# Kernel tuning notes

Measured on AMD Instinct MI355X. Metric: run time of the kernel, lower is better.

The kernel has to match this reference:

```python
import jax, jax.numpy as jnp
from jax import lax
import numpy as np

# ----- static optical constants (from config) -----
N = 500            # phase mask grid
PX = 1e-6          # pixel pitch [m]
WL = 532e-9        # wavelength [m]
FL = 0.1           # focal length [m]
RI = 1.0           # refractive index
FWHC = 150e-6      # laser beam FWHC
K = 2.0 * np.pi * RI / WL
QE, DARK_MEAN, READ_STD, GAIN, MAX_ADU = 0.9, 0.005, 1.6, 2.0, 65535.0
MAX_VAL = 4.0e9    # Normalize01 max
PHOTONS = 1.0e6    # photons per emitter (max_intensity-style scaling)
R = 15             # psf_keep_radius -> 31x31 crops

_x = np.arange(-N // 2, N // 2) * PX
_X, _Y = np.meshgrid(_x, _x)
INCIDENT = np.exp(-(_X**2 + _Y**2) / (2.0 * FWHC**2)).astype(np.float32)
_C1 = (np.pi / (WL * FL) * (_X**2 + _Y**2)) % (2.0 * np.pi)
B1 = np.exp(-1j * _C1).astype(np.complex64)
# angular-spectrum gamma, directly in unshifted fft order
_F = np.fft.fftfreq(N, d=PX)
_A, _B = np.meshgrid(RI * WL * _F, RI * WL * _F)
GAMMA = np.sqrt(np.maximum(1.0 - _A**2 - _B**2, 0.0)).astype(np.float32)

def _gauss7():
    m = (7 - 1) / 2.0
    y, x = np.ogrid[-m:m + 1, -m:m + 1]
    h = np.exp(-(x * x + y * y) / 2.0)
    h[h < np.finfo(h.dtype).eps * h.max()] = 0
    return h.astype(np.float32)
GAUSS7 = _gauss7()


def setup_inputs() -> dict:
    key = jax.random.key(0)
    k1, k2, k3, k4, k5, k6, k7 = jax.random.split(key, 7)
    B, Ne = 8, 64
    phase_mask = jax.random.uniform(k1, (N, N), jnp.float32, 0.0, 2.0 * np.pi)
    zs = jax.random.uniform(k2, (Ne,), jnp.float32, 0.0, 1e-4)  # defocus depths [m]
    xyz = jax.random.randint(k3, (B, Ne, 2), 0, 170, jnp.int32) + 15  # in [15,184]
    std_u = jax.random.uniform(k4, (1,), jnp.float32)
    eps_dark = jax.random.normal(k5, (B, 1, 198, 198), jnp.float32)
    eps_photon = jax.random.normal(k6, (B, 1, 198, 198), jnp.float32)
    eps_read = jax.random.normal(k7, (B, 1, 198, 198), jnp.float32)
    return {"phase_mask": phase_mask, "zs": zs, "xyz": xyz, "std_u": std_u,
            "eps_dark": eps_dark, "eps_photon": eps_photon, "eps_read": eps_read}


def _forward(phase_mask, zs, xyz, std_u, eps_dark, eps_photon, eps_read):
    Bn, Ne = xyz.shape[0], xyz.shape[1]
    # --- FFT-based PSF generation (angular spectrum propagation) ---
    field = (INCIDENT * jnp.exp(1j * phase_mask) * B1).astype(jnp.complex64)  # [N,N]
    Ef = jnp.fft.fft2(field)                                                  # [N,N]
    H = jnp.exp(1j * ((K * GAMMA)[None] * zs[:, None, None]))                 # [Ne,N,N]
    Eprop = jnp.fft.ifft2(Ef[None] * H)                                       # [Ne,N,N]
    inten = jnp.abs(Eprop) ** 2
    c = N // 2
    psf = inten[:, c - R:c + R + 1, c - R:c + R + 1]                          # [Ne,31,31]
    psf = psf / (jnp.sum(psf, (-2, -1), keepdims=True) + 1e-12) * PHOTONS
    images4D = jnp.broadcast_to(psf[None], (Bn, Ne, 2 * R + 1, 2 * R + 1))
    # --- imgs4dto3d: scatter-add 31x31 patches into 200x200 canvas ---
    offs = jnp.arange(2 * R + 1) - R
    rows = xyz[..., 0][..., None, None] + offs[None, None, :, None]           # [B,Ne,31,1]
    cols = xyz[..., 1][..., None, None] + offs[None, None, None, :]           # [B,Ne,1,31]
    bidx = jnp.arange(Bn)[:, None, None, None]
    canvas = jnp.zeros((Bn, 200, 200), psf.dtype).at[bidx, rows, cols].add(images4D)
    img = canvas[:, None]                                                     # [B,1,200,200]
    # --- BlurLayer: per-draw std gaussian, conv pad=2 -> 198x198 ---
    std = 0.8 + 0.4 * std_u[0]
    s2 = std * std
    kern = (1.0 / (2.0 * jnp.pi * s2)) * GAUSS7 ** (1.0 / s2)
    blurred = lax.conv_general_dilated(img, kern[None, None], (1, 1),
                                       [(2, 2), (2, 2)],
                                       dimension_numbers=("NCHW", "OIHW", "NCHW"))
    # --- NoiseLayer (reparameterized gaussian approximations) ---
    sig = blurred * QE
    dark = DARK_MEAN + eps_dark * jnp.sqrt(jnp.float32(DARK_MEAN))
    total = jnp.maximum(sig + dark, 0.0)
    noisy = total + eps_photon * jnp.sqrt(jnp.maximum(total, 1e-12))
    elec = noisy + eps_read * READ_STD
    adu = jnp.clip(elec * GAIN, 0.0, MAX_ADU)
    # --- Normalize01 ---
    out = jnp.where(adu <= 10.0, 1.0, jnp.minimum(adu, MAX_VAL)) / MAX_VAL
    return out.astype(jnp.float32)


def reference(phase_mask, zs, xyz, std_u, eps_dark, eps_photon, eps_read):
    return _forward(phase_mask, zs, xyz, std_u, eps_dark, eps_photon, eps_read)
```

## Files before the change

kernel.cpp:

```cpp
#include <hip/hip_runtime.h>
#include <math.h>

#define NN 500
#define NE 64
#define BATCH 8
#define RR 15
#define PW 31
#define CAN 200
#define OHW 198
#define TWO_PI_F 6.28318530717958647692f
#define SETUP_N (BATCH * CAN * CAN + NE + 49)

#define BG2_F16 (64 * 2 * 2 * 64 * 8)
#define ASCALE (1.0f / 64.0f)

using f16x8 = __attribute__((ext_vector_type(8))) _Float16;
using f32x16 = __attribute__((ext_vector_type(16))) float;

__device__ __forceinline__ void fast_sincos_red(float theta, float* s, float* c) {
    const float INV2PI = 0.15915494309189535f;
    const float PI2_HI = 6.28318548202514648f;
    const float PI2_LO = -1.7484556e-7f;
    float n = rintf(theta * INV2PI);
    float r = fmaf(n, -PI2_HI, theta);
    r = fmaf(n, -PI2_LO, r);
    *s = __sinf(r);
    *c = __cosf(r);
}

__global__ void k_setup(const float* __restrict__ std_u,
                        float* __restrict__ kgamma,
                        float2* __restrict__ tw,
                        float* __restrict__ kern,
                        float* __restrict__ canvas,
                        float* __restrict__ psf_sums,
                        _Float16* __restrict__ Bg2) {
    int idx = blockIdx.x * blockDim.x + threadIdx.x;
    if (idx < NN) {
        double th = 2.0 * M_PI * (double)idx / (double)NN;
        tw[idx] = make_float2((float)cos(th), (float)sin(th));
    }
    if (idx < BG2_F16) {
        int e = idx & 7;
        int lane = (idx >> 3) & 63;
        int nt = (idx >> 9) & 1;
        int plane = (idx >> 10) & 1;
        int gs = idx >> 11;
        int kap = gs * 16 + (lane >> 5) * 8 + e;
        int nu = nt * 32 + (lane & 31);
        float outv = 0.f;
        if (kap < 2 * NN) {
            int u = kap >> 1, p = kap & 1;
            int ri = nu >> 1, q = nu & 1;
            int r = 235 + ri;
            int m = (u * r) % NN;
            double th = 2.0 * M_PI * (double)m / (double)NN;
            double wre = cos(th), wim = sin(th);
            double val = (q == 0) ? ((p == 0) ? wre : -wim)
                                  : ((p == 0) ? wim : wre);
            float x = (float)val;
            _Float16 h = (_Float16)x;
            outv = (plane == 0) ? (float)h : (x - (float)h);
        }
        Bg2[idx] = (_Float16)outv;
    }
    if (idx < BATCH * CAN * CAN) canvas[idx] = 0.f;
    if (idx >= BATCH * CAN * CAN && idx < BATCH * CAN * CAN + NE)
        psf_sums[idx - BATCH * CAN * CAN] = 0.f;
    if (idx >= BATCH * CAN * CAN + NE && idx < SETUP_N) {
        int t = idx - (BATCH * CAN * CAN + NE);
        float stdv = 0.8f + 0.4f * std_u[0];
        float s2 = stdv * stdv;
        int a = t / 7 - 3, b = t % 7 - 3;
        float g = (float)exp(-0.5 * (double)(a * a + b * b));
        kern[t] = (1.0f / (2.0f * (float)M_PI * s2)) * powf(g, 1.0f / s2);
    }
    if (idx >= NN * NN) return;
    int i = idx / NN, j = idx % NN;
    double fy = (double)((i < 250) ? i : i - 500) * 2000.0;
    double fx = (double)((j < 250) ? j : j - 500) * 2000.0;
    double a = 5.32e-7 * fx;
    double b = 5.32e-7 * fy;
    double g = 1.0 - a * a - b * b;
    g = (g > 0.0) ? sqrt(g) : 0.0;
    float Kf = (float)(2.0 * M_PI * 1.0 / 5.32e-7);
    kgamma[idx] = Kf * (float)g;
}

__device__ __forceinline__ void ct_dft_stages(const float2* xs, const float2* tts,
                                              float2* S, int t,
                                              float2* out1, float2* out2, int* kout) {
    if (t < 250) {
        int d = t / 25;
        int b = t % 25;
        float2 st = tts[(25 * d) % NN];
        float wr = 1.f, wi = 0.f;
        float Er = 0.f, Ei = 0.f, Or_ = 0.f, Oi = 0.f;
#pragma unroll
        for (int a = 0; a < 20; a += 2) {
            float2 x0 = xs[25 * a + b];
            Er += x0.x * wr - x0.y * wi;
            Ei += x0.x * wi + x0.y * wr;
            float nr = wr * st.x - wi * st.y;
            float ni = wr * st.y + wi * st.x;
            float2 x1 = xs[25 * (a + 1) + b];
            Or_ += x1.x * nr - x1.y * ni;
            Oi  += x1.x * ni + x1.y * nr;
            wr = nr * st.x - ni * st.y;
            wi = nr * st.y + ni * st.x;
        }
        S[b * 21 + d]      = make_float2(Er + Or_, Ei + Oi);
        S[b * 21 + d + 10] = make_float2(Er - Or_, Ei - Oi);
    }
    __syncthreads();
    if (t < 250) {
        int k = t;
        int d1 = k % 20;
        int d2 = (d1 + 10) % 20;
        float2 s1 = tts[k];
        float wr = 1.f, wi = 0.f;
        float a1r = 0.f, a1i = 0.f, a2r = 0.f, a2i = 0.f;
#pragma unroll
        for (int b = 0; b < 25; ++b) {
            float2 u1 = S[b * 21 + d1];
            float2 u2 = S[b * 21 + d2];
            a1r += u1.x * wr - u1.y * wi;
            a1i += u1.x * wi + u1.y * wr;
            float sgnb = (b & 1) ? -1.f : 1.f;
            float w2r = sgnb * wr, w2i = sgnb * wi;
            a2r += u2.x * w2r - u2.y * w2i;
            a2i += u2.x * w2i + u2.y * w2r;
            float nr = wr * s1.x - wi * s1.y;
            wi = wr * s1.y + wi * s1.x;
            wr = nr;
        }
        *out1 = make_float2(a1r, a1i);
        *out2 = make_float2(a2r, a2i);
        *kout = k;
    }
}

__global__ void k_dft_rows(const float* __restrict__ phase, float2* __restrict__ dst,
                           const float2* __restrict__ tw) {
    __shared__ __align__(16) float2 xs[NN];
    __shared__ float2 tts[NN];
    __shared__ float2 S[25 * 21];
    int line = blockIdx.x;
    int t = threadIdx.x;
    const float INV2SIG = 2.2222222e7f;
    const float C1M = (float)(M_PI / 5.32e-8);
    float y = (float)(line - 250) * 1e-6f;
    float y2 = y * y;
    const float* prow = phase + (size_t)line * NN;
    for (int n = t; n < NN; n += 256) {
        float x = (float)(n - 250) * 1e-6f;
        float r2 = x * x + y2;
        float inc = __expf(-r2 * INV2SIG);
        float c1 = C1M * r2;
        float b1r = __cosf(c1), b1i = -__sinf(c1);
        float ph = prow[n];
        float sp = __sinf(ph), cp = __cosf(ph);
        float ar = inc * cp, ai = inc * sp;
        xs[n] = make_float2(ar * b1r - ai * b1i, ar * b1i + ai * b1r);
        float2 tt = tw[n];
        tts[n] = make_float2(tt.x, -tt.y);
    }
    __syncthreads();
    float2 o1, o2; int k;
    ct_dft_stages(xs, tts, S, t, &o1, &o2, &k);
    if (t < 250) {
        dst[(size_t)k * NN + line] = o1;
        dst[(size_t)(k + 250) * NN + line] = o2;
    }
}

__global__ void k_dft_cols(const float2* __restrict__ src, float2* __restrict__ dst,
                           const float2* __restrict__ tw) {
    __shared__ __align__(16) float2 xs[NN];
    __shared__ float2 tts[NN];
    __shared__ float2 S[25 * 21];
    int line = blockIdx.x;
    const float2* s = src + (size_t)line * NN;
    int t = threadIdx.x;
    for (int n = t; n < NN; n += 256) {
        xs[n] = s[n];
        float2 tt = tw[n];
        tts[n] = make_float2(tt.x, -tt.y);
    }
    __syncthreads();
    float2 o1, o2; int k;
    ct_dft_stages(xs, tts, S, t, &o1, &o2, &k);
    if (t < 250) {
        float2* dp = dst + (size_t)line * NN;
        dp[k] = o1;
        dp[k + 250] = o2;
    }
}

__global__ void __launch_bounds__(256)
k_prop_mfma(const float2* __restrict__ EfT,
            const float* __restrict__ kgamma,
            const float* __restrict__ zs,
            const _Float16* __restrict__ Bg2,
            float* __restrict__ part) {
    __shared__ __align__(16) float2 eft[512];
    __shared__ __align__(16) float kgs[512];
    __shared__ __align__(16) float ctile[64 * 64];

    int v = blockIdx.x;
    int t = threadIdx.x;
    int w = t >> 6;
    int wh = w >> 1;
    int mw = w & 1;
    int lane = t & 63;
    int l31 = lane & 31;
    int lk = lane >> 5;

    for (int n = t; n < 512; n += 256) {
        if (n < NN) {
            float2 e = EfT[(size_t)v * NN + n];
            eft[n] = make_float2(e.x * ASCALE, e.y * ASCALE);
            kgs[n] = kgamma[(size_t)v * NN + n];
        } else {
            eft[n] = make_float2(0.f, 0.f);
            kgs[n] = 0.f;
        }
    }
    float zv = zs[mw * 32 + l31];
    __syncthreads();

    f32x16 acc[2] = {};

#define MODSPLIT(ex, ey, kgv, i0) do {                                        \
        float s_, c_;                                                         \
        fast_sincos_red((kgv) * zv, &s_, &c_);                                \
        float yr = (ex) * c_ - (ey) * s_;                                     \
        float yi = (ex) * s_ + (ey) * c_;                                     \
        _Float16 h0 = (_Float16)yr;                                           \
        ah[i0] = h0; al[i0] = (_Float16)(yr - (float)h0);                     \
        _Float16 h1 = (_Float16)yi;                                           \
        ah[i0 + 1] = h1; al[i0 + 1] = (_Float16)(yi - (float)h1);             \
    } while (0)

    const _Float16* bbase = Bg2 + (size_t)(wh * 32) * 2048 + (size_t)lane * 8;
#pragma unroll 4
    for (int s = 0; s < 32; ++s) {
        const _Float16* bs = bbase + (size_t)s * 2048;
        f16x8 bh0 = *(const f16x8*)(bs);
        f16x8 bh1 = *(const f16x8*)(bs + 512);
        f16x8 bl0 = *(const f16x8*)(bs + 1024);
        f16x8 bl1 = *(const f16x8*)(bs + 1536);
        int u0 = wh * 256 + s * 8 + lk * 4;
        f16x8 ah, al;
        {
            float4 e01 = *(const float4*)&eft[u0];
            float4 e23 = *(const float4*)&eft[u0 + 2];
            float4 kg4 = *(const float4*)&kgs[u0];
            MODSPLIT(e01.x, e01.y, kg4.x, 0);
            MODSPLIT(e01.z, e01.w, kg4.y, 2);
            MODSPLIT(e23.x, e23.y, kg4.z, 4);
            MODSPLIT(e23.z, e23.w, kg4.w, 6);
        }
        acc[0] = __builtin_amdgcn_mfma_f32_32x32x16_f16(ah, bh0, acc[0], 0, 0, 0);
        acc[0] = __builtin_amdgcn_mfma_f32_32x32x16_f16(al, bh0, acc[0], 0, 0, 0);
        acc[0] = __builtin_amdgcn_mfma_f32_32x32x16_f16(ah, bl0, acc[0], 0, 0, 0);
        acc[1] = __builtin_amdgcn_mfma_f32_32x32x16_f16(ah, bh1, acc[1], 0, 0, 0);
        acc[1] = __builtin_amdgcn_mfma_f32_32x32x16_f16(al, bh1, acc[1], 0, 0, 0);
        acc[1] = __builtin_amdgcn_mfma_f32_32x32x16_f16(ah, bl1, acc[1], 0, 0, 0);
    }
#undef MODSPLIT

    if (wh == 0) {
#pragma unroll
        for (int nt = 0; nt < 2; ++nt)
#pragma unroll
            for (int reg = 0; reg < 16; ++reg) {
                int row = (reg & 3) + 8 * (reg >> 2) + 4 * lk;
                ctile[(mw * 32 + row) * 64 + nt * 32 + l31] = acc[nt][reg];
            }
    }
    __syncthreads();
    if (wh == 1) {
#pragma unroll
        for (int nt = 0; nt < 2; ++nt)
#pragma unroll
            for (int reg = 0; reg < 16; ++reg) {
                int row = (reg & 3) + 8 * (reg >> 2) + 4 * lk;
                ctile[(mw * 32 + row) * 64 + nt * 32 + l31] += acc[nt][reg];
            }
    }
    __syncthreads();
#pragma unroll
    for (int p = 0; p < 4; ++p) {
        int idx = p * 256 + t;
        int z = idx >> 4, c4 = idx & 15;
        float4 val = *(const float4*)&ctile[z * 64 + c4 * 4];
        *(float4*)&part[((size_t)z * NN + v) * 64 + c4 * 4] = val;
    }
}

__global__ void k_prop_cols(const float* __restrict__ part,
                            float* __restrict__ psf,
                            float* __restrict__ psf_sums) {
    __shared__ __align__(16) float X2[NN][16];
    int rq = blockIdx.x;
    int z  = blockIdx.y;
    int t  = threadIdx.x;
    const float* p0 = part + ((size_t)z * NN) * 64 + rq * 16;
    for (int i = t; i < NN * 4; i += 256) {
        int v = i >> 2, q4 = i & 3;
        float4 a = *(const float4*)(p0 + (size_t)v * 64 + q4 * 4);
        *(float4*)&X2[v][q4 * 4] = a;
    }
    __syncthreads();
    int ril = t >> 5;
    int ri  = rq * 8 + ril;
    int ci  = t & 31;
    float val = 0.f;
    if (ri < PW && ci < PW) {
        int c = 235 + ci;
        float ar = 0.f, ai = 0.f;
        float sr, si;
        {
            float th = (TWO_PI_F / NN) * (float)(c % NN);
            sincosf(th, &si, &sr);
        }
        for (int vb = 0; vb < 4; ++vb) {
            int v0 = vb * 125;
            float wr, wi;
            float th = (TWO_PI_F / NN) * (float)((v0 * c) % NN);
            sincosf(th, &wi, &wr);
            for (int v = v0; v < v0 + 125; ++v) {
                float2 xy = *(const float2*)&X2[v][2 * ril];
                ar += xy.x * wr - xy.y * wi;
                ai += xy.x * wi + xy.y * wr;
                float nwr = wr * sr - wi * si;
                wi = wr * si + wi * sr;
                wr = nwr;
            }
        }
        const float inv = 64.0f / 250000.0f;
        float re = ar * inv, im = ai * inv;
        val = re * re + im * im;
        psf[(size_t)z * (PW * PW) + ri * PW + ci] = val;
    }
#pragma unroll
    for (int m = 1; m < 64; m <<= 1) val += __shfl_xor(val, m);
    if ((t & 63) == 0) atomicAdd(&psf_sums[z], val);
}

__global__ void k_scatter(const float* __restrict__ psf,
                          const float* __restrict__ psf_sums,
                          const int* __restrict__ xyz,
                          float* __restrict__ canvas) {
    int e = blockIdx.x;
    int b = blockIdx.y;
    int r0 = xyz[(b * NE + e) * 2 + 0] - RR;
    int c0 = xyz[(b * NE + e) * 2 + 1] - RR;
    float sc = 1.0e6f / (psf_sums[e] + 1e-12f);
    float* cb = canvas + (size_t)b * (CAN * CAN);
    for (int p = threadIdx.x; p < PW * PW; p += blockDim.x) {
        int i = p / PW, j = p % PW;
        atomicAdd(cb + (r0 + i) * CAN + (c0 + j), psf[e * PW * PW + p] * sc);
    }
}

__global__ void k_final(const float* __restrict__ canvas,
                        const float* __restrict__ kern,
                        const float* __restrict__ eps_dark,
                        const float* __restrict__ eps_photon,
                        const float* __restrict__ eps_read,
                        float* __restrict__ out) {
    __shared__ float kk[49];
    __shared__ float tile[14][40];
    int b = blockIdx.z;
    int tx = threadIdx.x, ty = threadIdx.y;
    int t = ty * 32 + tx;
    int j0 = blockIdx.x * 32, i0 = blockIdx.y * 8;
    if (t < 49) kk[t] = kern[t];
    const float* cb = canvas + (size_t)b * (CAN * CAN);
    for (int p = t; p < 14 * 38; p += 256) {
        int rr = p / 38, cc = p % 38;
        int gi = i0 + rr - 2, gj = j0 + cc - 2;
        tile[rr][cc] = (gi >= 0 && gi < CAN && gj >= 0 && gj < CAN)
                           ? cb[gi * CAN + gj] : 0.f;
    }
    __syncthreads();
    int i = i0 + ty, j = j0 + tx;
    if (i >= OHW || j >= OHW) return;
    float acc = 0.f;
#pragma unroll
    for (int a = 0; a < 7; ++a)
#pragma unroll
        for (int q = 0; q < 7; ++q)
            acc += tile[ty + a][tx + q] * kk[a * 7 + q];
    int idx = b * (OHW * OHW) + i * OHW + j;
    float sig = acc * 0.9f;
    float dark = 0.005f + eps_dark[idx] * sqrtf(0.005f);
    float total = fmaxf(sig + dark, 0.0f);
    float noisy = total + eps_photon[idx] * sqrtf(fmaxf(total, 1e-12f));
    float elec = noisy + eps_read[idx] * 1.6f;
    float adu = fminf(fmaxf(elec * 2.0f, 0.0f), 65535.0f);
    float v = (adu <= 10.0f) ? 1.0f : fminf(adu, 4.0e9f);
    out[idx] = v / 4.0e9f;
}

extern "C" void kernel_launch(void* const* d_in, const int* in_sizes, int n_in,
                              void* d_out, int out_size, void* d_ws, size_t ws_size,
                              hipStream_t stream) {
    const float* phase    = (const float*)d_in[0];
    const float* zs       = (const float*)d_in[1];
    const int*   xyz      = (const int*)d_in[2];
    const float* std_u    = (const float*)d_in[3];
    const float* epsd     = (const float*)d_in[4];
    const float* epsp     = (const float*)d_in[5];
    const float* epsr     = (const float*)d_in[6];
    float* out = (float*)d_out;

    char* ws = (char*)d_ws;
    size_t off = 0;
    auto alloc = [&](size_t bytes) {
        off = (off + 255) & ~(size_t)255;
        size_t o = off; off += bytes; return o;
    };
    float*  kgamma   = (float*) (ws + alloc((size_t)NN * NN * 4));
    float2* tw       = (float2*)(ws + alloc((size_t)NN * 8));
    float2* R1T      = (float2*)(ws + alloc((size_t)NN * NN * 8));
    float2* EfT      = (float2*)(ws + alloc((size_t)NN * NN * 8));
    float*  part     = (float*) (ws + alloc((size_t)NE * NN * 64 * 4));
    float*  psf      = (float*) (ws + alloc((size_t)NE * PW * PW * 4));
    float*  psf_sums = (float*) (ws + alloc((size_t)NE * 4));
    float*  kern     = (float*) (ws + alloc((size_t)64 * 4));
    float*  canvas   = (float*) (ws + alloc((size_t)BATCH * CAN * CAN * 4));
    _Float16* Bg2    = (_Float16*)(ws + alloc((size_t)BG2_F16 * 2));
    (void)ws_size; (void)n_in; (void)in_sizes; (void)out_size;

    k_setup<<<(SETUP_N + 255) / 256, 256, 0, stream>>>(
        std_u, kgamma, tw, kern, canvas, psf_sums, Bg2);
    k_dft_rows<<<NN, 256, 0, stream>>>(phase, R1T, tw);
    k_dft_cols<<<NN, 256, 0, stream>>>(R1T, EfT, tw);
    k_prop_mfma<<<NN, 256, 0, stream>>>(EfT, kgamma, zs, Bg2, part);
    k_prop_cols<<<dim3(4, NE), 256, 0, stream>>>(part, psf, psf_sums);
    k_scatter<<<dim3(NE, BATCH), 256, 0, stream>>>(psf, psf_sums, xyz, canvas);
    k_final<<<dim3((OHW + 31) / 32, (OHW + 7) / 8, BATCH), dim3(32, 8), 0, stream>>>(
        canvas, kern, epsd, epsp, epsr, out);
}
```

Measured before the change: 137.4 us.

## Split prop MFMA over z halves and four-way K split across waves

```diff
diff --git a/kernel.cpp b/kernel.cpp
--- a/kernel.cpp
+++ b/kernel.cpp
@@ -203,15 +203,15 @@
             const float* __restrict__ zs,
             const _Float16* __restrict__ Bg2,
             float* __restrict__ part) {
-    __shared__ __align__(16) float2 eft[512];
-    __shared__ __align__(16) float kgs[512];
-    __shared__ __align__(16) float ctile[64 * 64];
+    __shared__ __align__(16) char smem[4 * 2048 * 4];
+    float2* eft = (float2*)smem;
+    float*  kgs = (float*)(smem + 4096);
+    float*  ctile4 = (float*)smem;
 
     int v = blockIdx.x;
+    int zh = blockIdx.y;
     int t = threadIdx.x;
     int w = t >> 6;
-    int wh = w >> 1;
-    int mw = w & 1;
     int lane = t & 63;
     int l31 = lane & 31;
     int lk = lane >> 5;
@@ -226,7 +226,7 @@
             kgs[n] = 0.f;
         }
     }
-    float zv = zs[mw * 32 + l31];
+    float zv = zs[zh * 32 + l31];
     __syncthreads();
 
     f32x16 acc[2] = {};
@@ -242,15 +242,15 @@
         ah[i0 + 1] = h1; al[i0 + 1] = (_Float16)(yi - (float)h1);             \
     } while (0)
 
-    const _Float16* bbase = Bg2 + (size_t)(wh * 32) * 2048 + (size_t)lane * 8;
+    const _Float16* bbase = Bg2 + (size_t)(w * 16) * 2048 + (size_t)lane * 8;
 #pragma unroll 4
-    for (int s = 0; s < 32; ++s) {
+    for (int s = 0; s < 16; ++s) {
         const _Float16* bs = bbase + (size_t)s * 2048;
         f16x8 bh0 = *(const f16x8*)(bs);
         f16x8 bh1 = *(const f16x8*)(bs + 512);
         f16x8 bl0 = *(const f16x8*)(bs + 1024);
         f16x8 bl1 = *(const f16x8*)(bs + 1536);
-        int u0 = wh * 256 + s * 8 + lk * 4;
+        int u0 = w * 128 + s * 8 + lk * 4;
         f16x8 ah, al;
         {
             float4 e01 = *(const float4*)&eft[u0];
@@ -270,32 +270,32 @@
     }
 #undef MODSPLIT
 
-    if (wh == 0) {
+    __syncthreads();
+    {
+        float* slice = ctile4 + w * 2048;
 #pragma unroll
         for (int nt = 0; nt < 2; ++nt)
 #pragma unroll
             for (int reg = 0; reg < 16; ++reg) {
                 int row = (reg & 3) + 8 * (reg >> 2) + 4 * lk;
-                ctile[(mw * 32 + row) * 64 + nt * 32 + l31] = acc[nt][reg];
+                slice[row * 64 + nt * 32 + l31] = acc[nt][reg];
             }
     }
     __syncthreads();
-    if (wh == 1) {
-#pragma unroll
-        for (int nt = 0; nt < 2; ++nt)
-#pragma unroll
-            for (int reg = 0; reg < 16; ++reg) {
-                int row = (reg & 3) + 8 * (reg >> 2) + 4 * lk;
-                ctile[(mw * 32 + row) * 64 + nt * 32 + l31] += acc[nt][reg];
-            }
-    }
-    __syncthreads();
-#pragma unroll
-    for (int p = 0; p < 4; ++p) {
-        int idx = p * 256 + t;
-        int z = idx >> 4, c4 = idx & 15;
-        float4 val = *(const float4*)&ctile[z * 64 + c4 * 4];
-        *(float4*)&part[((size_t)z * NN + v) * 64 + c4 * 4] = val;
+#pragma unroll
+    for (int pass = 0; pass < 2; ++pass) {
+        int idx = pass * 256 + t;
+        int i4 = idx * 4;
+        int z = i4 >> 6, c4 = (i4 & 63) >> 2;
+        float4 a0 = *(const float4*)&ctile4[i4];
+        float4 a1 = *(const float4*)&ctile4[2048 + i4];
+        float4 a2 = *(const float4*)&ctile4[4096 + i4];
+        float4 a3 = *(const float4*)&ctile4[6144 + i4];
+        float4 val = make_float4(a0.x + a1.x + a2.x + a3.x,
+                                 a0.y + a1.y + a2.y + a3.y,
+                                 a0.z + a1.z + a2.z + a3.z,
+                                 a0.w + a1.w + a2.w + a3.w);
+        *(float4*)&part[((size_t)(zh * 32 + z) * NN + v) * 64 + c4 * 4] = val;
     }
 }
 
@@ -439,7 +439,7 @@
         std_u, kgamma, tw, kern, canvas, psf_sums, Bg2);
     k_dft_rows<<<NN, 256, 0, stream>>>(phase, R1T, tw);
     k_dft_cols<<<NN, 256, 0, stream>>>(R1T, EfT, tw);
-    k_prop_mfma<<<NN, 256, 0, stream>>>(EfT, kgamma, zs, Bg2, part);
+    k_prop_mfma<<<dim3(NN, 2), 256, 0, stream>>>(EfT, kgamma, zs, Bg2, part);
     k_prop_cols<<<dim3(4, NE), 256, 0, stream>>>(part, psf, psf_sums);
     k_scatter<<<dim3(NE, BATCH), 256, 0, stream>>>(psf, psf_sums, xyz, canvas);
     k_final<<<dim3((OHW + 31) / 32, (OHW + 7) / 8, BATCH), dim3(32, 8), 0, stream>>>(
```

After: 136.4 us. No clear change (-0.7%).
